# Performance work log

Measured on AMD Instinct MI355X. Metric: run time of the kernel, lower is better.

The kernel has to match this reference:

```python
import jax, jax.numpy as jnp
import numpy as np

D_IN = 2048
D_OUT = 2048
NUM_HEADS = 32
NUM_KV_GROUPS = 8
HEAD_DIM = D_OUT // NUM_HEADS          # 64
GROUP_SIZE = NUM_HEADS // NUM_KV_GROUPS  # 4
BATCH = 2
SEQ = 2048


def _rope(x, cos, sin):
    # x: [b, h, s, d]; cos/sin: [s, d]
    d = x.shape[-1]
    x1, x2 = x[..., : d // 2], x[..., d // 2:]
    rotated = jnp.concatenate((-x2, x1), axis=-1)
    return x * cos[None, None, :, :] + rotated * sin[None, None, :, :]


def setup_inputs() -> dict:
    key = jax.random.key(0)
    ks = jax.random.split(key, 8)
    x = jax.random.normal(ks[0], (BATCH, SEQ, D_IN), dtype=jnp.float32)
    cos = jax.random.normal(ks[1], (SEQ, HEAD_DIM), dtype=jnp.float32)
    sin = jax.random.normal(ks[2], (SEQ, HEAD_DIM), dtype=jnp.float32)
    # causal mask: True above the diagonal = masked out
    mask = jnp.triu(jnp.ones((SEQ, SEQ), dtype=jnp.bool_), k=1)
    s = 0.02
    Wq = jax.random.normal(ks[3], (D_IN, D_OUT), dtype=jnp.float32) * s
    Wk = jax.random.normal(ks[4], (D_IN, NUM_KV_GROUPS * HEAD_DIM), dtype=jnp.float32) * s
    Wv = jax.random.normal(ks[5], (D_IN, NUM_KV_GROUPS * HEAD_DIM), dtype=jnp.float32) * s
    Wo = jax.random.normal(ks[6], (D_OUT, D_OUT), dtype=jnp.float32) * s
    return {"x": x, "cos": cos, "sin": sin, "mask": mask,
            "Wq": Wq, "Wk": Wk, "Wv": Wv, "Wo": Wo}


def reference(x, cos, sin, mask, Wq, Wk, Wv, Wo):
    b, s, _ = x.shape
    # projections (Linear, no bias): weights stored as [d_in, d_out]
    q = (x @ Wq).reshape(b, s, NUM_HEADS, HEAD_DIM).transpose(0, 2, 1, 3)      # [b,H,s,d]
    k = (x @ Wk).reshape(b, s, NUM_KV_GROUPS, HEAD_DIM).transpose(0, 2, 1, 3)  # [b,G,s,d]
    v = (x @ Wv).reshape(b, s, NUM_KV_GROUPS, HEAD_DIM).transpose(0, 2, 1, 3)  # [b,G,s,d]
    q = _rope(q, cos, sin)
    k = _rope(k, cos, sin)
    # GQA broadcast: repeat each KV group group_size times along head axis
    k = jnp.repeat(k, GROUP_SIZE, axis=1)  # [b,H,s,d]
    v = jnp.repeat(v, GROUP_SIZE, axis=1)  # [b,H,s,d]
    scores = jnp.einsum('bhqd,bhkd->bhqk', q, k)
    scores = jnp.where(mask[None, None, :, :], -jnp.inf, scores)
    # original scales AFTER masking: softmax(scores / sqrt(head_dim)); -inf stays -inf
    attn = jax.nn.softmax(scores * (1.0 / np.sqrt(HEAD_DIM)), axis=-1)
    ctx = jnp.einsum('bhqk,bhkd->bqhd', attn, v).reshape(b, s, D_OUT)
    return ctx @ Wo
```

## Files before the change

kernel.cpp:

```cpp
#include <hip/hip_runtime.h>
#include <hip/hip_fp16.h>

#define SEQ    2048
#define DIN    2048
#define DOUT   2048
#define NH     32
#define NKV    8
#define HD     64
#define BB     2

typedef _Float16 half_t;
typedef __attribute__((ext_vector_type(8))) _Float16 half8;
typedef __attribute__((ext_vector_type(4))) _Float16 half4;
typedef __attribute__((ext_vector_type(2))) __fp16   fp16x2;
typedef __attribute__((ext_vector_type(4))) float    floatx4;

union H8U { half8 h; int u[4]; };
union H2I { fp16x2 h; int i; };

#if __has_builtin(__builtin_amdgcn_exp2f)
#define EXP2F(x) __builtin_amdgcn_exp2f(x)
#else
#define EXP2F(x) __expf((x) * 0.6931471805599453f)
#endif

__device__ __forceinline__ void gload16(void* l, const void* g) {
    __builtin_amdgcn_global_load_lds(
        (const __attribute__((address_space(1))) void*)g,
        (__attribute__((address_space(3))) void*)l, 16, 0, 0);
}

__global__ void cast_f2h(const float* __restrict__ in, half_t* __restrict__ out, int n4) {
    int i = blockIdx.x * blockDim.x + threadIdx.x;
    if (i < n4) {
        float4 v = ((const float4*)in)[i];
        half4 h;
        h[0] = (half_t)v.x; h[1] = (half_t)v.y; h[2] = (half_t)v.z; h[3] = (half_t)v.w;
        ((half4*)out)[i] = h;
    }
}

__global__ __launch_bounds__(256) void tcast(const float* __restrict__ in, half_t* __restrict__ out,
                                             int Kd, int Nd) {
    __shared__ float T[32][33];
    int x0 = blockIdx.x * 32, y0 = blockIdx.y * 32;
    int tx = threadIdx.x & 31, ty = threadIdx.x >> 5;
    #pragma unroll
    for (int j = 0; j < 4; j++)
        T[ty + j * 8][tx] = in[(size_t)(y0 + ty + j * 8) * Nd + x0 + tx];
    __syncthreads();
    #pragma unroll
    for (int j = 0; j < 4; j++)
        out[(size_t)(x0 + ty + j * 8) * Kd + y0 + tx] = (half_t)T[tx][ty + j * 8];
}

__global__ __launch_bounds__(256) void gemm_qkv(
    const half_t* __restrict__ A, const half_t* __restrict__ Bt,
    const float* __restrict__ cosb, const float* __restrict__ sinb,
    half_t* __restrict__ Qh, half_t* __restrict__ Kh, half_t* __restrict__ Vt)
{
    __shared__ half_t As[4096];
    __shared__ half_t Bs[4096];
    const int K = DIN;
    int tid = threadIdx.x, wave = tid >> 6, lane = tid & 63;
    int quad = lane >> 4, l15 = lane & 15;
    int m0 = blockIdx.y * 128, n0 = blockIdx.x * 128;
    int wm = (wave >> 1) * 64, wn = (wave & 1) * 64;
    floatx4 acc[4][4] = {};

    int srow[2], skoff[2], sldso[2];
    #pragma unroll
    for (int is = 0; is < 2; is++) {
        int s = is * 256 + tid;
        int p = s >> 3, sc = s & 7;
        int c = sc ^ (p & 7);
        srow[is]  = 2 * p + (c >> 2);
        skoff[is] = (c & 3) * 8;
        sldso[is] = (is * 256 + wave * 64) * 8;
    }
    for (int k0 = 0; k0 < K; k0 += 32) {
        __syncthreads();
        #pragma unroll
        for (int is = 0; is < 2; is++) {
            gload16(&As[sldso[is]], A  + (size_t)(m0 + srow[is]) * K + k0 + skoff[is]);
            gload16(&Bs[sldso[is]], Bt + (size_t)(n0 + srow[is]) * K + k0 + skoff[is]);
        }
        __syncthreads();
        half8 af[4], bf[4];
        #pragma unroll
        for (int i = 0; i < 4; i++) {
            int r = wm + i * 16 + l15, p = r >> 1;
            int sc = (((r & 1) * 4 + quad) ^ (p & 7));
            af[i] = *(const half8*)&As[p * 64 + sc * 8];
            int rn = wn + i * 16 + l15, pn = rn >> 1;
            int scn = (((rn & 1) * 4 + quad) ^ (pn & 7));
            bf[i] = *(const half8*)&Bs[pn * 64 + scn * 8];
        }
        #pragma unroll
        for (int i = 0; i < 4; i++)
            #pragma unroll
            for (int j = 0; j < 4; j++)
                acc[i][j] = __builtin_amdgcn_mfma_f32_16x16x32_f16(af[i], bf[j], acc[i][j], 0, 0, 0);
    }

    const int headg = (n0 + wn) >> 6;
    const int b = m0 >> 11;
    const int s_base = (m0 & 2047) + wm + quad * 4;

    if (headg < 32) {
        half_t* outp = Qh + (size_t)(b * NH + headg) * SEQ * 64;
        #pragma unroll
        for (int i = 0; i < 4; i++)
            #pragma unroll
            for (int j = 0; j < 4; j++) {
                int d = j * 16 + l15;
                #pragma unroll
                for (int r = 0; r < 4; r++)
                    outp[(size_t)(s_base + i * 16 + r) * 64 + d] = (half_t)acc[i][j][r];
            }
    } else if (headg < 40) {
        half_t* outp = Kh + (size_t)(b * NKV + (headg - 32)) * SEQ * 64;
        #pragma unroll
        for (int i = 0; i < 4; i++)
            #pragma unroll
            for (int r = 0; r < 4; r++) {
                int s = s_base + i * 16 + r;
                #pragma unroll
                for (int j = 0; j < 2; j++) {
                    int d = j * 16 + l15;
                    float x1 = acc[i][j][r], x2 = acc[i][j + 2][r];
                    float c1 = cosb[s * 64 + d],      s1 = sinb[s * 64 + d];
                    float c2 = cosb[s * 64 + d + 32], s2 = sinb[s * 64 + d + 32];
                    outp[(size_t)s * 64 + d]      = (half_t)(x1 * c1 - x2 * s1);
                    outp[(size_t)s * 64 + d + 32] = (half_t)(x2 * c2 + x1 * s2);
                }
            }
    } else {
        half_t* vtp = Vt + (size_t)(b * NKV + (headg - 40)) * 64 * SEQ;
        #pragma unroll
        for (int i = 0; i < 4; i++) {
            int s = s_base + i * 16;
            #pragma unroll
            for (int j = 0; j < 4; j++) {
                int d = j * 16 + l15;
                half4 hv;
                hv[0] = (half_t)acc[i][j][0];
                hv[1] = (half_t)acc[i][j][1];
                hv[2] = (half_t)acc[i][j][2];
                hv[3] = (half_t)acc[i][j][3];
                *(half4*)(vtp + (size_t)d * SEQ + s) = hv;
            }
        }
    }
}

__global__ __launch_bounds__(256) void gemm_tn_f(
    const half_t* __restrict__ A, const half_t* __restrict__ Bt,
    float* __restrict__ C, int M, int N, int K)
{
    __shared__ half_t As[4096];
    __shared__ half_t Bs[4096];
    int tid = threadIdx.x, wave = tid >> 6, lane = tid & 63;
    int quad = lane >> 4, l15 = lane & 15;
    int m0 = blockIdx.y * 128, n0 = blockIdx.x * 128;
    int wm = (wave >> 1) * 64, wn = (wave & 1) * 64;
    floatx4 acc[4][4] = {};
    int srow[2], skoff[2], sldso[2];
    #pragma unroll
    for (int is = 0; is < 2; is++) {
        int s = is * 256 + tid;
        int p = s >> 3, sc = s & 7;
        int c = sc ^ (p & 7);
        srow[is]  = 2 * p + (c >> 2);
        skoff[is] = (c & 3) * 8;
        sldso[is] = (is * 256 + wave * 64) * 8;
    }
    for (int k0 = 0; k0 < K; k0 += 32) {
        __syncthreads();
        #pragma unroll
        for (int is = 0; is < 2; is++) {
            gload16(&As[sldso[is]], A  + (size_t)(m0 + srow[is]) * K + k0 + skoff[is]);
            gload16(&Bs[sldso[is]], Bt + (size_t)(n0 + srow[is]) * K + k0 + skoff[is]);
        }
        __syncthreads();
        half8 af[4], bf[4];
        #pragma unroll
        for (int i = 0; i < 4; i++) {
            int r = wm + i * 16 + l15, p = r >> 1;
            int sc = (((r & 1) * 4 + quad) ^ (p & 7));
            af[i] = *(const half8*)&As[p * 64 + sc * 8];
            int rn = wn + i * 16 + l15, pn = rn >> 1;
            int scn = (((rn & 1) * 4 + quad) ^ (pn & 7));
            bf[i] = *(const half8*)&Bs[pn * 64 + scn * 8];
        }
        #pragma unroll
        for (int i = 0; i < 4; i++)
            #pragma unroll
            for (int j = 0; j < 4; j++)
                acc[i][j] = __builtin_amdgcn_mfma_f32_16x16x32_f16(af[i], bf[j], acc[i][j], 0, 0, 0);
    }
    #pragma unroll
    for (int i = 0; i < 4; i++) {
        int row = m0 + wm + i * 16 + quad * 4;
        #pragma unroll
        for (int j = 0; j < 4; j++) {
            int col = n0 + wn + j * 16 + l15;
            #pragma unroll
            for (int r = 0; r < 4; r++)
                C[(size_t)(row + r) * N + col] = acc[i][j][r];
        }
    }
}

__global__ __launch_bounds__(256, 4) void attn(
    const half_t* __restrict__ Qh, const half_t* __restrict__ Kh,
    const half_t* __restrict__ Vt, const float* __restrict__ cosb,
    const float* __restrict__ sinb, half_t* __restrict__ ctx)
{
    __shared__ half_t Ks[2][4096];
    __shared__ half_t Vs[2][4096];

    const int tid = threadIdx.x, wave = tid >> 6, lane = tid & 63;
    const int quad = lane >> 4, l15 = lane & 15;
    const int bid = blockIdx.x;
    const int k  = bid >> 8;
    const int u  = bid & 255;
    const int q2 = u & 3;
    const int bh = u >> 2;
    const int qt = (k == 0) ? 15 - 2 * q2 : (k == 1) ? 2 * q2
                 : (k == 2) ? 14 - 2 * q2 : 2 * q2 + 1;
    const int b  = bh >> 5;
    const int h  = bh & 31;
    const int g  = h >> 2;
    const int q0 = qt * 128;
    const int wm = wave * 32;

    const half_t* kp = Kh + (size_t)(b * NKV + g) * SEQ * 64;
    const half_t* vp = Vt + (size_t)(b * NKV + g) * 64 * SEQ;

    half8 qf[2][2];
    {
        const float sc = 0.125f * 1.44269504088896f;
        const half_t* qpp = Qh + ((size_t)(b * NH + h) * SEQ + q0 + wm) * 64;
        #pragma unroll
        for (int mf = 0; mf < 2; mf++) {
            int s = q0 + wm + mf * 16 + l15;
            const float* cp = cosb + s * 64 + quad * 8;
            const float* sp = sinb + s * 64 + quad * 8;
            half8 xa = *(const half8*)(qpp + (size_t)(mf * 16 + l15) * 64 + quad * 8);
            half8 xb = *(const half8*)(qpp + (size_t)(mf * 16 + l15) * 64 + 32 + quad * 8);
            float4 c1a = *(const float4*)(cp),      c1b = *(const float4*)(cp + 4);
            float4 s1a = *(const float4*)(sp),      s1b = *(const float4*)(sp + 4);
            float4 c2a = *(const float4*)(cp + 32), c2b = *(const float4*)(cp + 36);
            float4 s2a = *(const float4*)(sp + 32), s2b = *(const float4*)(sp + 36);
            const float* c1 = (const float*)&c1a;
            #pragma unroll
            for (int t = 0; t < 8; t++) {
                float cc1 = (t < 4) ? ((const float*)&c1a)[t] : ((const float*)&c1b)[t - 4];
                float ss1 = (t < 4) ? ((const float*)&s1a)[t] : ((const float*)&s1b)[t - 4];
                float cc2 = (t < 4) ? ((const float*)&c2a)[t] : ((const float*)&c2b)[t - 4];
                float ss2 = (t < 4) ? ((const float*)&s2a)[t] : ((const float*)&s2b)[t - 4];
                float x1 = (float)xa[t], x2 = (float)xb[t];
                qf[mf][0][t] = (half_t)((x1 * cc1 - x2 * ss1) * sc);
                qf[mf][1][t] = (half_t)((x2 * cc2 + x1 * ss2) * sc);
            }
            (void)c1;
        }
    }

    int koff[2], voff[2], lo[2];
    #pragma unroll
    for (int is = 0; is < 2; is++) {
        int s = is * 256 + tid;
        int p = s >> 3, c = (s & 7) ^ (p & 7);
        koff[is] = p * 64 + c * 8;
        voff[is] = p * SEQ + c * 8;
        lo[is]   = (is * 256 + wave * 64) * 8;
    }

    float m_i[2], l_i[2];
    m_i[0] = m_i[1] = -__builtin_inff();
    l_i[0] = l_i[1] = 0.f;
    floatx4 o[2][4] = {};

    const int ntiles = 2 * qt + 2;
    #pragma unroll
    for (int is = 0; is < 2; is++) {
        gload16(&Ks[0][lo[is]], kp + koff[is]);
        gload16(&Vs[0][lo[is]], vp + voff[is]);
    }

    const int srcA = l15 + ((quad & 1) ? 32 : 0);
    const int srcB = srcA + 16;
    const bool hiK = (quad >> 1) != 0;

    for (int kt = 0; kt < ntiles; kt++) {
        const int cur = kt & 1;
        const int kb  = kt * 64;
        __syncthreads();
        if (kt + 1 < ntiles) {
            const int kb2 = (kt + 1) * 64;
            #pragma unroll
            for (int is = 0; is < 2; is++) {
                gload16(&Ks[cur ^ 1][lo[is]], kp + (size_t)kb2 * 64 + koff[is]);
                gload16(&Vs[cur ^ 1][lo[is]], vp + kb2 + voff[is]);
            }
        }

        if (kb <= q0 + wm + 31) {
            floatx4 sa[2][4] = {};
            #pragma unroll
            for (int kc = 0; kc < 2; kc++)
                #pragma unroll
                for (int kf = 0; kf < 4; kf++) {
                    int row = kf * 16 + l15;
                    int sc = ((kc * 4 + quad) ^ (row & 7));
                    half8 kfr = *(const half8*)&Ks[cur][row * 64 + sc * 8];
                    sa[0][kf] = __builtin_amdgcn_mfma_f32_16x16x32_f16(kfr, qf[0][kc], sa[0][kf], 0, 0, 0);
                    sa[1][kf] = __builtin_amdgcn_mfma_f32_16x16x32_f16(kfr, qf[1][kc], sa[1][kf], 0, 0, 0);
                }

            if (kb + 63 > q0 + wm) {
                #pragma unroll
                for (int kf = 0; kf < 4; kf++)
                    #pragma unroll
                    for (int r = 0; r < 4; r++) {
                        int key = kb + kf * 16 + quad * 4 + r;
                        if (key > q0 + wm + l15)      sa[0][kf][r] = -__builtin_inff();
                        if (key > q0 + wm + 16 + l15) sa[1][kf][r] = -__builtin_inff();
                    }
            }

            int eh[2][4][2];
            float alpha[2];
            #pragma unroll
            for (int mf = 0; mf < 2; mf++) {
                float mt = sa[mf][0][0];
                #pragma unroll
                for (int kf = 0; kf < 4; kf++)
                    #pragma unroll
                    for (int r = 0; r < 4; r++) mt = fmaxf(mt, sa[mf][kf][r]);
                mt = fmaxf(mt, __shfl_xor(mt, 16));
                mt = fmaxf(mt, __shfl_xor(mt, 32));
                float mn = fmaxf(m_i[mf], mt);
                alpha[mf] = EXP2F(m_i[mf] - mn);
                m_i[mf] = mn;
                float rs = 0.f;
                #pragma unroll
                for (int kf = 0; kf < 4; kf++) {
                    float e0 = EXP2F(sa[mf][kf][0] - mn);
                    float e1 = EXP2F(sa[mf][kf][1] - mn);
                    float e2 = EXP2F(sa[mf][kf][2] - mn);
                    float e3 = EXP2F(sa[mf][kf][3] - mn);
                    rs += (e0 + e1) + (e2 + e3);
                    H2I p01, p23;
                    p01.h = __builtin_amdgcn_cvt_pkrtz(e0, e1);
                    p23.h = __builtin_amdgcn_cvt_pkrtz(e2, e3);
                    eh[mf][kf][0] = p01.i;
                    eh[mf][kf][1] = p23.i;
                }
                rs += __shfl_xor(rs, 16);
                rs += __shfl_xor(rs, 32);
                l_i[mf] = l_i[mf] * alpha[mf] + rs;
                #pragma unroll
                for (int nf = 0; nf < 4; nf++)
                    #pragma unroll
                    for (int r = 0; r < 4; r++) o[mf][nf][r] *= alpha[mf];
            }

            #pragma unroll
            for (int kc = 0; kc < 2; kc++) {
                H8U pf[2];
                #pragma unroll
                for (int mf = 0; mf < 2; mf++) {
                    int a0 = __shfl(eh[mf][2 * kc][0],     srcA);
                    int a1 = __shfl(eh[mf][2 * kc][1],     srcA);
                    int b0 = __shfl(eh[mf][2 * kc + 1][0], srcA);
                    int b1 = __shfl(eh[mf][2 * kc + 1][1], srcA);
                    int c0 = __shfl(eh[mf][2 * kc][0],     srcB);
                    int c1 = __shfl(eh[mf][2 * kc][1],     srcB);
                    int d0 = __shfl(eh[mf][2 * kc + 1][0], srcB);
                    int d1 = __shfl(eh[mf][2 * kc + 1][1], srcB);
                    pf[mf].u[0] = hiK ? b0 : a0;
                    pf[mf].u[1] = hiK ? b1 : a1;
                    pf[mf].u[2] = hiK ? d0 : c0;
                    pf[mf].u[3] = hiK ? d1 : c1;
                }
                #pragma unroll
                for (int nf = 0; nf < 4; nf++) {
                    int row = nf * 16 + l15;
                    int sc = ((kc * 4 + quad) ^ (row & 7));
                    half8 vf = *(const half8*)&Vs[cur][row * 64 + sc * 8];
                    o[0][nf] = __builtin_amdgcn_mfma_f32_16x16x32_f16(vf, pf[0].h, o[0][nf], 0, 0, 0);
                    o[1][nf] = __builtin_amdgcn_mfma_f32_16x16x32_f16(vf, pf[1].h, o[1][nf], 0, 0, 0);
                }
            }
        }
    }

    #pragma unroll
    for (int mf = 0; mf < 2; mf++) {
        float inv = 1.0f / l_i[mf];
        int s = q0 + wm + mf * 16 + l15;
        half_t* op = ctx + (size_t)(b * SEQ + s) * DOUT + h * 64 + quad * 4;
        #pragma unroll
        for (int nf = 0; nf < 4; nf++) {
            half4 hv;
            hv[0] = (half_t)(o[mf][nf][0] * inv);
            hv[1] = (half_t)(o[mf][nf][1] * inv);
            hv[2] = (half_t)(o[mf][nf][2] * inv);
            hv[3] = (half_t)(o[mf][nf][3] * inv);
            *(half4*)(op + nf * 16) = hv;
        }
    }
}

extern "C" void kernel_launch(void* const* d_in, const int* in_sizes, int n_in,
                              void* d_out, int out_size, void* d_ws, size_t ws_size,
                              hipStream_t stream) {
    const float* x    = (const float*)d_in[0];
    const float* cosb = (const float*)d_in[1];
    const float* sinb = (const float*)d_in[2];
    const float* Wq   = (const float*)d_in[4];
    const float* Wk   = (const float*)d_in[5];
    const float* Wv   = (const float*)d_in[6];
    const float* Wo   = (const float*)d_in[7];
    float* out = (float*)d_out;

    const size_t M  = (size_t)BB * SEQ;
    const size_t nX = M * DIN;

    char* ws = (char*)d_ws;
    const size_t MB = 1048576;
    half_t* xh     = (half_t*)(ws);
    half_t* WqkvT  = (half_t*)(ws + 16 * MB);
    half_t* WoT    = (half_t*)(ws + 28 * MB);
    half_t* Qh     = (half_t*)(ws + 36 * MB);
    half_t* Kh     = (half_t*)(ws + 52 * MB);
    half_t* Vt     = (half_t*)(ws + 56 * MB);
    half_t* ctxh   = (half_t*)(ws + 60 * MB);

    cast_f2h<<<(nX / 4) / 256, 256, 0, stream>>>(x, xh, nX / 4);
    tcast<<<dim3(64, 64), 256, 0, stream>>>(Wq, WqkvT, DIN, DOUT);
    tcast<<<dim3(16, 64), 256, 0, stream>>>(Wk, WqkvT + (size_t)2048 * 2048, DIN, 512);
    tcast<<<dim3(16, 64), 256, 0, stream>>>(Wv, WqkvT + (size_t)2560 * 2048, DIN, 512);
    tcast<<<dim3(64, 64), 256, 0, stream>>>(Wo, WoT, DOUT, DOUT);

    gemm_qkv<<<dim3(3072 / 128, M / 128), 256, 0, stream>>>(xh, WqkvT, cosb, sinb, Qh, Kh, Vt);

    attn<<<BB * NH * (SEQ / 128), 256, 0, stream>>>(Qh, Kh, Vt, cosb, sinb, ctxh);

    gemm_tn_f<<<dim3(DOUT / 128, M / 128), 256, 0, stream>>>(ctxh, WoT, out, M, DOUT, DIN);
}
```

Baseline: 359.4 us.

## Double-buffer LDS tiles in both GEMMs and merge weight transpose launches

Both fp16 GEMM kernels now use two LDS buffers, so the global-to-LDS load for the next K-step is issued before computing on the current one. This drops one barrier per iteration and overlaps memory latency with MFMA work. The four weight transpose/cast launches are merged into one kernel that picks the matrix from the block index, cutting launch overhead. The cost is doubled LDS per block (32KB), which may lower occupancy.

```diff
diff --git a/kernel.cpp b/kernel.cpp
--- a/kernel.cpp
+++ b/kernel.cpp
@@ -40,10 +40,19 @@
     }
 }
 
-__global__ __launch_bounds__(256) void tcast(const float* __restrict__ in, half_t* __restrict__ out,
-                                             int Kd, int Nd) {
+__global__ __launch_bounds__(256) void tcast_all(
+    const float* __restrict__ Wq, const float* __restrict__ Wk,
+    const float* __restrict__ Wv, const float* __restrict__ Wo,
+    half_t* __restrict__ WqkvT, half_t* __restrict__ WoT)
+{
     __shared__ float T[32][33];
-    int x0 = blockIdx.x * 32, y0 = blockIdx.y * 32;
+    int id = blockIdx.x;
+    const float* in; half_t* out; int Nd, xt;
+    if (id < 4096)       { in = Wq; out = WqkvT;                          Nd = 2048; xt = id & 63; id >>= 6; }
+    else if (id < 5120)  { id -= 4096; in = Wk; out = WqkvT + (size_t)2048 * 2048; Nd = 512; xt = id & 15; id >>= 4; }
+    else if (id < 6144)  { id -= 5120; in = Wv; out = WqkvT + (size_t)2560 * 2048; Nd = 512; xt = id & 15; id >>= 4; }
+    else                 { id -= 6144; in = Wo; out = WoT;                Nd = 2048; xt = id & 63; id >>= 6; }
+    int x0 = xt * 32, y0 = id * 32;
     int tx = threadIdx.x & 31, ty = threadIdx.x >> 5;
     #pragma unroll
     for (int j = 0; j < 4; j++)
@@ -51,7 +60,7 @@
     __syncthreads();
     #pragma unroll
     for (int j = 0; j < 4; j++)
-        out[(size_t)(x0 + ty + j * 8) * Kd + y0 + tx] = (half_t)T[tx][ty + j * 8];
+        out[(size_t)(x0 + ty + j * 8) * 2048 + y0 + tx] = (half_t)T[tx][ty + j * 8];
 }
 
 __global__ __launch_bounds__(256) void gemm_qkv(
@@ -59,9 +68,9 @@
     const float* __restrict__ cosb, const float* __restrict__ sinb,
     half_t* __restrict__ Qh, half_t* __restrict__ Kh, half_t* __restrict__ Vt)
 {
-    __shared__ half_t As[4096];
-    __shared__ half_t Bs[4096];
-    const int K = DIN;
+    __shared__ half_t As[2][4096];
+    __shared__ half_t Bs[2][4096];
+    const int K = DIN, NIT = DIN / 32;
     int tid = threadIdx.x, wave = tid >> 6, lane = tid & 63;
     int quad = lane >> 4, l15 = lane & 15;
     int m0 = blockIdx.y * 128, n0 = blockIdx.x * 128;
@@ -78,23 +87,31 @@
         skoff[is] = (c & 3) * 8;
         sldso[is] = (is * 256 + wave * 64) * 8;
     }
-    for (int k0 = 0; k0 < K; k0 += 32) {
+    #pragma unroll
+    for (int is = 0; is < 2; is++) {
+        gload16(&As[0][sldso[is]], A  + (size_t)(m0 + srow[is]) * K + skoff[is]);
+        gload16(&Bs[0][sldso[is]], Bt + (size_t)(n0 + srow[is]) * K + skoff[is]);
+    }
+    for (int kk = 0; kk < NIT; kk++) {
+        const int cur = kk & 1;
         __syncthreads();
-        #pragma unroll
-        for (int is = 0; is < 2; is++) {
-            gload16(&As[sldso[is]], A  + (size_t)(m0 + srow[is]) * K + k0 + skoff[is]);
-            gload16(&Bs[sldso[is]], Bt + (size_t)(n0 + srow[is]) * K + k0 + skoff[is]);
-        }
-        __syncthreads();
+        if (kk + 1 < NIT) {
+            int k0 = (kk + 1) * 32;
+            #pragma unroll
+            for (int is = 0; is < 2; is++) {
+                gload16(&As[cur ^ 1][sldso[is]], A  + (size_t)(m0 + srow[is]) * K + k0 + skoff[is]);
+                gload16(&Bs[cur ^ 1][sldso[is]], Bt + (size_t)(n0 + srow[is]) * K + k0 + skoff[is]);
+            }
+        }
         half8 af[4], bf[4];
         #pragma unroll
         for (int i = 0; i < 4; i++) {
             int r = wm + i * 16 + l15, p = r >> 1;
             int sc = (((r & 1) * 4 + quad) ^ (p & 7));
-            af[i] = *(const half8*)&As[p * 64 + sc * 8];
+            af[i] = *(const half8*)&As[cur][p * 64 + sc * 8];
             int rn = wn + i * 16 + l15, pn = rn >> 1;
             int scn = (((rn & 1) * 4 + quad) ^ (pn & 7));
-            bf[i] = *(const half8*)&Bs[pn * 64 + scn * 8];
+            bf[i] = *(const half8*)&Bs[cur][pn * 64 + scn * 8];
         }
         #pragma unroll
         for (int i = 0; i < 4; i++)
@@ -158,8 +175,9 @@
     const half_t* __restrict__ A, const half_t* __restrict__ Bt,
     float* __restrict__ C, int M, int N, int K)
 {
-    __shared__ half_t As[4096];
-    __shared__ half_t Bs[4096];
+    __shared__ half_t As[2][4096];
+    __shared__ half_t Bs[2][4096];
+    const int NIT = 2048 / 32;
     int tid = threadIdx.x, wave = tid >> 6, lane = tid & 63;
     int quad = lane >> 4, l15 = lane & 15;
     int m0 = blockIdx.y * 128, n0 = blockIdx.x * 128;
@@ -175,23 +193,31 @@
         skoff[is] = (c & 3) * 8;
         sldso[is] = (is * 256 + wave * 64) * 8;
     }
-    for (int k0 = 0; k0 < K; k0 += 32) {
+    #pragma unroll
+    for (int is = 0; is < 2; is++) {
+        gload16(&As[0][sldso[is]], A  + (size_t)(m0 + srow[is]) * K + skoff[is]);
+        gload16(&Bs[0][sldso[is]], Bt + (size_t)(n0 + srow[is]) * K + skoff[is]);
+    }
+    for (int kk = 0; kk < NIT; kk++) {
+        const int cur = kk & 1;
         __syncthreads();
-        #pragma unroll
-        for (int is = 0; is < 2; is++) {
-            gload16(&As[sldso[is]], A  + (size_t)(m0 + srow[is]) * K + k0 + skoff[is]);
-            gload16(&Bs[sldso[is]], Bt + (size_t)(n0 + srow[is]) * K + k0 + skoff[is]);
-        }
-        __syncthreads();
+        if (kk + 1 < NIT) {
+            int k0 = (kk + 1) * 32;
+            #pragma unroll
+            for (int is = 0; is < 2; is++) {
+                gload16(&As[cur ^ 1][sldso[is]], A  + (size_t)(m0 + srow[is]) * K + k0 + skoff[is]);
+                gload16(&Bs[cur ^ 1][sldso[is]], Bt + (size_t)(n0 + srow[is]) * K + k0 + skoff[is]);
+            }
+        }
         half8 af[4], bf[4];
         #pragma unroll
         for (int i = 0; i < 4; i++) {
             int r = wm + i * 16 + l15, p = r >> 1;
             int sc = (((r & 1) * 4 + quad) ^ (p & 7));
-            af[i] = *(const half8*)&As[p * 64 + sc * 8];
+            af[i] = *(const half8*)&As[cur][p * 64 + sc * 8];
             int rn = wn + i * 16 + l15, pn = rn >> 1;
             int scn = (((rn & 1) * 4 + quad) ^ (pn & 7));
-            bf[i] = *(const half8*)&Bs[pn * 64 + scn * 8];
+            bf[i] = *(const half8*)&Bs[cur][pn * 64 + scn * 8];
         }
         #pragma unroll
         for (int i = 0; i < 4; i++)
@@ -253,7 +279,6 @@
             float4 s1a = *(const float4*)(sp),      s1b = *(const float4*)(sp + 4);
             float4 c2a = *(const float4*)(cp + 32), c2b = *(const float4*)(cp + 36);
             float4 s2a = *(const float4*)(sp + 32), s2b = *(const float4*)(sp + 36);
-            const float* c1 = (const float*)&c1a;
             #pragma unroll
             for (int t = 0; t < 8; t++) {
                 float cc1 = (t < 4) ? ((const float*)&c1a)[t] : ((const float*)&c1b)[t - 4];
@@ -264,7 +289,6 @@
                 qf[mf][0][t] = (half_t)((x1 * cc1 - x2 * ss1) * sc);
                 qf[mf][1][t] = (half_t)((x2 * cc2 + x1 * ss2) * sc);
             }
-            (void)c1;
         }
     }
 
@@ -441,10 +465,7 @@
     half_t* ctxh   = (half_t*)(ws + 60 * MB);
 
     cast_f2h<<<(nX / 4) / 256, 256, 0, stream>>>(x, xh, nX / 4);
-    tcast<<<dim3(64, 64), 256, 0, stream>>>(Wq, WqkvT, DIN, DOUT);
-    tcast<<<dim3(16, 64), 256, 0, stream>>>(Wk, WqkvT + (size_t)2048 * 2048, DIN, 512);
-    tcast<<<dim3(16, 64), 256, 0, stream>>>(Wv, WqkvT + (size_t)2560 * 2048, DIN, 512);
-    tcast<<<dim3(64, 64), 256, 0, stream>>>(Wo, WoT, DOUT, DOUT);
+    tcast_all<<<10240, 256, 0, stream>>>(Wq, Wk, Wv, Wo, WqkvT, WoT);
 
     gemm_qkv<<<dim3(3072 / 128, M / 128), 256, 0, stream>>>(xh, WqkvT, cosb, sinb, Qh, Kh, Vt);
 
```

After: 373.9 us. 1.04x slower.
